# Optimization experiments

Hardware: AMD Instinct MI355X
Metric: run time of the kernel (lower is better)

The kernel has to match this reference:

```python
import jax, jax.numpy as jnp
import numpy as np

EMBED_DIM = 1024
NUM_HEADS = 16
HEAD_DIM = EMBED_DIM // NUM_HEADS


def setup_inputs() -> dict:
    key = jax.random.key(0)
    ks = jax.random.split(key, 9)
    B, N, C = 2, 2048, EMBED_DIM
    s = 1.0 / np.sqrt(C)
    x = jax.random.normal(ks[0], (B, N, C), dtype=jnp.float32)
    Wq = jax.random.uniform(ks[1], (C, C), jnp.float32, -s, s)
    bq = jax.random.uniform(ks[2], (C,), jnp.float32, -s, s)
    Wk = jax.random.uniform(ks[3], (C, C), jnp.float32, -s, s)
    bk = jax.random.uniform(ks[4], (C,), jnp.float32, -s, s)
    Wv = jax.random.uniform(ks[5], (C, C), jnp.float32, -s, s)
    bv = jax.random.uniform(ks[6], (C,), jnp.float32, -s, s)
    Wo = jax.random.uniform(ks[7], (C, C), jnp.float32, -s, s)
    bo = jax.random.uniform(ks[8], (C,), jnp.float32, -s, s)
    return {"x": x, "Wq": Wq, "bq": bq, "Wk": Wk, "bk": bk,
            "Wv": Wv, "bv": bv, "Wo": Wo, "bo": bo}


def reference(x, Wq, bq, Wk, bk, Wv, bv, Wo, bo):
    B, N, C = x.shape
    H, D = NUM_HEADS, HEAD_DIM
    # projections: weights stored as [in, out] (torch Linear applies x @ W.T; here W already transposed)
    q = (x @ Wq + bq).reshape(B, N, H, D).transpose(0, 2, 1, 3)  # [B,H,N,D]
    k = (x @ Wk + bk).reshape(B, N, H, D).transpose(0, 2, 1, 3)
    v = (x @ Wv + bv).reshape(B, N, H, D).transpose(0, 2, 1, 3)
    scores = jnp.einsum('bhnd,bhmd->bhnm', q, k) / jnp.sqrt(jnp.float32(D))
    w = jax.nn.softmax(scores, axis=-1)
    out = jnp.einsum('bhnm,bhmd->bhnd', w, v)  # [B,H,N,D]
    out = out.transpose(0, 2, 1, 3).reshape(B, N, C)
    return out @ Wo + bo
```

## Files before the change

### kernel.cpp

```cpp
#include <hip/hip_runtime.h>

typedef short short4v __attribute__((ext_vector_type(4)));
typedef short short8 __attribute__((ext_vector_type(8)));
typedef unsigned uint4v __attribute__((ext_vector_type(4)));
typedef float floatx4 __attribute__((ext_vector_type(4)));
typedef float floatx16 __attribute__((ext_vector_type(16)));

#define SEQ 2048
#define CDIM 1024
#define NH 16
#define HD 64

__device__ __forceinline__ short f2bf(float f){
  unsigned u = __builtin_bit_cast(unsigned, f);
  u += 0x7fff + ((u >> 16) & 1);
  return (short)(u >> 16);
}
__device__ __forceinline__ float fexp2(float x){
  float r; asm("v_exp_f32 %0, %1" : "=v"(r) : "v"(x)); return r;
}
__device__ __forceinline__ int swz(int row, int k){
  return row*64 + ((((k >> 3) ^ row) & 7) << 3) + (k & 7);
}
__device__ __forceinline__ void gload16(const short* g, short* l){
  __builtin_amdgcn_global_load_lds(
      (const __attribute__((address_space(1))) void*)g,
      (__attribute__((address_space(3))) void*)l, 16, 0, 0);
}

struct PrepArgs { const float* w[4]; short* wT[4]; const float* x; short* xb; };
__global__ __launch_bounds__(256) void prep(PrepArgs pa){
  int z = blockIdx.z, tid = threadIdx.x;
  if(z >= 4){
    int blk = (z-4)*256 + blockIdx.y*16 + blockIdx.x;
    int i = (blk*256 + tid) * 4;
    float4 v = *(const float4*)&pa.x[i];
    short4v o = { f2bf(v.x), f2bf(v.y), f2bf(v.z), f2bf(v.w) };
    *(short4v*)&pa.xb[i] = o;
    return;
  }
  const float* __restrict__ in = pa.w[z];
  short* __restrict__ out = pa.wT[z];
  __shared__ short t[64][68];
  int r0 = blockIdx.y * 64, c0 = blockIdx.x * 64;
  #pragma unroll
  for(int i=0;i<4;i++){
    int id = tid + i*256;
    int r = id >> 4, c4 = (id & 15) * 4;
    float4 v = *(const float4*)&in[(long long)(r0+r)*CDIM + c0 + c4];
    t[r][c4]   = f2bf(v.x); t[r][c4+1] = f2bf(v.y);
    t[r][c4+2] = f2bf(v.z); t[r][c4+3] = f2bf(v.w);
  }
  __syncthreads();
  #pragma unroll
  for(int i=0;i<4;i++){
    int id = tid + i*256;
    int c = id >> 4, r4 = (id & 15) * 4;
    short4v o = { t[r4][c], t[r4+1][c], t[r4+2][c], t[r4+3][c] };
    *(short4v*)&out[(long long)(c0+c)*CDIM + r0 + r4] = o;
  }
}

__global__ __launch_bounds__(256) void transpose64(
    const short* __restrict__ in, short* __restrict__ out,
    long long zs_in, long long zs_out, int ld_in, int ld_out){
  in  += (long long)blockIdx.z * zs_in;
  out += (long long)blockIdx.z * zs_out;
  __shared__ short t[64][72];
  int r0 = blockIdx.y * 64, c0 = blockIdx.x * 64, tid = threadIdx.x;
  #pragma unroll
  for(int i=0;i<2;i++){
    int id = tid + i*256;
    int r = id >> 3, c8 = (id & 7) * 8;
    short8 x = *(const short8*)&in[(long long)(r0+r)*ld_in + c0 + c8];
    #pragma unroll
    for(int j=0;j<8;j++) t[r][c8+j] = x[j];
  }
  __syncthreads();
  #pragma unroll
  for(int i=0;i<2;i++){
    int id = tid + i*256;
    int c = id >> 3, r8 = (id & 7) * 8;
    short8 x;
    #pragma unroll
    for(int j=0;j<8;j++) x[j] = t[r8+j][c];
    *(short8*)&out[(long long)(c0+c)*ld_out + r0 + r8] = x;
  }
}

struct GemmArgs {
  const short* X;
  const short* Wt[3];
  const float* bias[3];
  void* out[3];
  float scale[3];
  int mode;
};

__global__ __launch_bounds__(256,4) void gemm128(GemmArgs ga){
  int z = blockIdx.z;
  const short* __restrict__ X  = ga.X;
  const short* __restrict__ Wt = ga.Wt[z];
  const float* __restrict__ bi = ga.bias[z];

  __shared__ __align__(16) short As[128*64];
  __shared__ __align__(16) short Bs[128*64];
  int tid = threadIdx.x, lane = tid & 63, w = tid >> 6;
  int m0 = blockIdx.x * 128, n0 = blockIdx.y * 128;
  int wr = (w >> 1) * 64, wc = (w & 1) * 64;
  int rsub = lane >> 3;
  int ksw  = (((lane & 7) ^ (lane >> 3)) & 7) << 3;

  const short* gA = X  + (long long)m0 * CDIM;
  const short* gB = Wt + (long long)n0 * CDIM;

  floatx4 acc[4][4];
  #pragma unroll
  for(int m=0;m<4;m++)
    #pragma unroll
    for(int n=0;n<4;n++) acc[m][n] = (floatx4){0.f,0.f,0.f,0.f};

  for(int kt=0; kt<CDIM; kt+=64){
    #pragma unroll
    for(int i=0;i<4;i++){
      int rr = (i*4+w)*8 + rsub;
      gload16(gA + (long long)rr*CDIM + kt + ksw, &As[(i*4+w)*512]);
      gload16(gB + (long long)rr*CDIM + kt + ksw, &Bs[(i*4+w)*512]);
    }
    __syncthreads();
    #pragma unroll
    for(int kk=0;kk<2;kk++){
      int kb = kk*32 + (lane>>4)*8;
      short8 af[4], bfq[4];
      #pragma unroll
      for(int m=0;m<4;m++) af[m]  = *(short8*)&As[swz(wr + m*16 + (lane&15), kb)];
      #pragma unroll
      for(int n=0;n<4;n++) bfq[n] = *(short8*)&Bs[swz(wc + n*16 + (lane&15), kb)];
      __builtin_amdgcn_s_setprio(1);
      #pragma unroll
      for(int m=0;m<4;m++)
        #pragma unroll
        for(int n=0;n<4;n++)
          acc[m][n] = __builtin_amdgcn_mfma_f32_16x16x32_bf16(af[m], bfq[n], acc[m][n], 0,0,0);
      __builtin_amdgcn_s_setprio(0);
    }
    __syncthreads();
  }

  #pragma unroll
  for(int m=0;m<4;m++){
    #pragma unroll
    for(int n=0;n<4;n++){
      int col = n0 + wc + n*16 + (lane & 15);
      float b = bi[col];
      #pragma unroll
      for(int j=0;j<4;j++){
        int row = m0 + wr + m*16 + (lane>>4)*4 + j;
        float r = acc[m][n][j] + b;
        if(ga.mode == 0){
          ((float*)ga.out[z])[(long long)row*CDIM + col] = r;
        } else {
          int bb = row >> 11, nn = row & 2047;
          int hh = col >> 6, dd = col & 63;
          ((short*)ga.out[z])[(long long)(((bb<<4)+hh)*SEQ + nn)*HD + dd] = f2bf(r * ga.scale[z]);
        }
      }
    }
  }
}

__global__ __launch_bounds__(512,4) void attn_fwd(
    const short* __restrict__ q, const short* __restrict__ k,
    const short* __restrict__ vT, short* __restrict__ ao){
  int bh = blockIdx.y;
  int b = bh >> 4, h = bh & 15;
  const short* Q = q  + (long long)bh * SEQ * HD;
  const short* K = k  + (long long)bh * SEQ * HD;
  const short* V = vT + (long long)bh * HD * SEQ;

  __shared__ __align__(16) short Kb[2][64*64];
  __shared__ __align__(16) short Vb[2][64*64];
  int tid = threadIdx.x, lane = tid & 63, w = tid >> 6;
  int wsub = w & 3, half = w >> 2;
  int l31 = lane & 31, hi = lane >> 5;
  int rsub = lane >> 3;
  int ksw  = (((lane & 7) ^ (lane >> 3)) & 7) << 3;
  int q0 = blockIdx.x * 128 + wsub * 32;
  int kvbase = half * (SEQ/2);

  short8 qf[4];
  {
    const short* qp = Q + (long long)(q0 + l31)*HD + hi*8;
    #pragma unroll
    for(int ks=0; ks<4; ks++) qf[ks] = *(const short8*)(qp + ks*16);
  }
  short8 onesf;
  #pragma unroll
  for(int j=0;j<8;j++) onesf[j] = (short)0x3F80;

  floatx16 accO0 = (floatx16)(0.f), accO1 = (floatx16)(0.f);
  floatx16 lacc  = (floatx16)(0.f);

  for(int t=0; t<16; t++){
    int kvn = kvbase + t*64;
    #pragma unroll
    for(int i=0;i<2;i++){
      int r = (i*4+wsub)*8 + rsub;
      gload16(K + (long long)(kvn + r)*HD + ksw, &Kb[half][(i*4+wsub)*512]);
      gload16(V + (long long)r*SEQ + kvn + ksw,  &Vb[half][(i*4+wsub)*512]);
    }
    __syncthreads();

    floatx16 s0 = (floatx16)(0.f), s1 = (floatx16)(0.f);
    __builtin_amdgcn_s_setprio(1);
    #pragma unroll
    for(int ks=0; ks<4; ks++){
      short8 kf0 = *(short8*)&Kb[half][swz(l31,      ks*16 + hi*8)];
      short8 kf1 = *(short8*)&Kb[half][swz(32 + l31, ks*16 + hi*8)];
      s0 = __builtin_amdgcn_mfma_f32_32x32x16_bf16(kf0, qf[ks], s0, 0,0,0);
      s1 = __builtin_amdgcn_mfma_f32_32x32x16_bf16(kf1, qf[ks], s1, 0,0,0);
    }
    __builtin_amdgcn_s_setprio(0);

    float p0[16], p1[16];
    #pragma unroll
    for(int r=0;r<16;r++){ p0[r] = fexp2(s0[r]); p1[r] = fexp2(s1[r]); }

    unsigned c0,c1,c2,c3,c4,c5,c6,c7, d0,d1,d2,d3,d4,d5,d6,d7;
    asm("v_cvt_pk_bf16_f32 %0, %1, %2" : "=v"(c0) : "v"(p0[0]),  "v"(p0[1]));
    asm("v_cvt_pk_bf16_f32 %0, %1, %2" : "=v"(c1) : "v"(p0[2]),  "v"(p0[3]));
    asm("v_cvt_pk_bf16_f32 %0, %1, %2" : "=v"(c2) : "v"(p0[4]),  "v"(p0[5]));
    asm("v_cvt_pk_bf16_f32 %0, %1, %2" : "=v"(c3) : "v"(p0[6]),  "v"(p0[7]));
    asm("v_cvt_pk_bf16_f32 %0, %1, %2" : "=v"(c4) : "v"(p0[8]),  "v"(p0[9]));
    asm("v_cvt_pk_bf16_f32 %0, %1, %2" : "=v"(c5) : "v"(p0[10]), "v"(p0[11]));
    asm("v_cvt_pk_bf16_f32 %0, %1, %2" : "=v"(c6) : "v"(p0[12]), "v"(p0[13]));
    asm("v_cvt_pk_bf16_f32 %0, %1, %2" : "=v"(c7) : "v"(p0[14]), "v"(p0[15]));
    asm("v_cvt_pk_bf16_f32 %0, %1, %2" : "=v"(d0) : "v"(p1[0]),  "v"(p1[1]));
    asm("v_cvt_pk_bf16_f32 %0, %1, %2" : "=v"(d1) : "v"(p1[2]),  "v"(p1[3]));
    asm("v_cvt_pk_bf16_f32 %0, %1, %2" : "=v"(d2) : "v"(p1[4]),  "v"(p1[5]));
    asm("v_cvt_pk_bf16_f32 %0, %1, %2" : "=v"(d3) : "v"(p1[6]),  "v"(p1[7]));
    asm("v_cvt_pk_bf16_f32 %0, %1, %2" : "=v"(d4) : "v"(p1[8]),  "v"(p1[9]));
    asm("v_cvt_pk_bf16_f32 %0, %1, %2" : "=v"(d5) : "v"(p1[10]), "v"(p1[11]));
    asm("v_cvt_pk_bf16_f32 %0, %1, %2" : "=v"(d6) : "v"(p1[12]), "v"(p1[13]));
    asm("v_cvt_pk_bf16_f32 %0, %1, %2" : "=v"(d7) : "v"(p1[14]), "v"(p1[15]));
    asm("v_permlane32_swap_b32 %0, %1" : "+v"(c0), "+v"(c2));
    asm("v_permlane32_swap_b32 %0, %1" : "+v"(c1), "+v"(c3));
    asm("v_permlane32_swap_b32 %0, %1" : "+v"(c4), "+v"(c6));
    asm("v_permlane32_swap_b32 %0, %1" : "+v"(c5), "+v"(c7));
    asm("v_permlane32_swap_b32 %0, %1" : "+v"(d0), "+v"(d2));
    asm("v_permlane32_swap_b32 %0, %1" : "+v"(d1), "+v"(d3));
    asm("v_permlane32_swap_b32 %0, %1" : "+v"(d4), "+v"(d6));
    asm("v_permlane32_swap_b32 %0, %1" : "+v"(d5), "+v"(d7));
    short8 pa[4];
    { uint4v u = {c0,c1,c2,c3}; pa[0] = __builtin_bit_cast(short8, u); }
    { uint4v u = {c4,c5,c6,c7}; pa[1] = __builtin_bit_cast(short8, u); }
    { uint4v u = {d0,d1,d2,d3}; pa[2] = __builtin_bit_cast(short8, u); }
    { uint4v u = {d4,d5,d6,d7}; pa[3] = __builtin_bit_cast(short8, u); }

    __builtin_amdgcn_s_setprio(1);
    #pragma unroll
    for(int ks=0; ks<4; ks++){
      short8 vf0 = *(short8*)&Vb[half][swz(l31,      ks*16 + hi*8)];
      short8 vf1 = *(short8*)&Vb[half][swz(32 + l31, ks*16 + hi*8)];
      accO0 = __builtin_amdgcn_mfma_f32_32x32x16_bf16(pa[ks], vf0, accO0, 0,0,0);
      accO1 = __builtin_amdgcn_mfma_f32_32x32x16_bf16(pa[ks], vf1, accO1, 0,0,0);
      lacc  = __builtin_amdgcn_mfma_f32_32x32x16_bf16(pa[ks], onesf, lacc, 0,0,0);
    }
    __builtin_amdgcn_s_setprio(0);

    __syncthreads();
  }

  float* Ko  = (float*)&Kb[0][0];
  float* VoS = (float*)&Vb[0][0];
  if(half == 1){
    #pragma unroll
    for(int r=0;r<16;r++){
      Ko [(wsub*16 + r)*64 + lane] = accO0[r];
      VoS[(wsub*16 + r)*64 + lane] = accO1[r];
    }
  }
  __syncthreads();
  if(half == 0){
    #pragma unroll
    for(int r=0;r<16;r++){
      accO0[r] += Ko [(wsub*16 + r)*64 + lane];
      accO1[r] += VoS[(wsub*16 + r)*64 + lane];
    }
  }
  __syncthreads();
  if(half == 1){
    #pragma unroll
    for(int r=0;r<16;r++) Ko[(wsub*16 + r)*64 + lane] = lacc[r];
  }
  __syncthreads();
  if(half == 0){
    #pragma unroll
    for(int r=0;r<16;r++){
      int qr = (r&3) + 8*(r>>2) + 4*hi;
      float lnew = lacc[r] + Ko[(wsub*16 + r)*64 + lane];
      float inv = 1.f / lnew;
      long long row = (long long)(b*SEQ + q0 + qr);
      ao[row*CDIM + h*HD + l31]      = f2bf(accO0[r] * inv);
      ao[row*CDIM + h*HD + 32 + l31] = f2bf(accO1[r] * inv);
    }
  }
}

extern "C" void kernel_launch(void* const* d_in, const int* in_sizes, int n_in,
                              void* d_out, int out_size, void* d_ws, size_t ws_size,
                              hipStream_t stream){
  const float* x  = (const float*)d_in[0];
  const float* Wq = (const float*)d_in[1];
  const float* bq = (const float*)d_in[2];
  const float* Wk = (const float*)d_in[3];
  const float* bk = (const float*)d_in[4];
  const float* Wv = (const float*)d_in[5];
  const float* bv = (const float*)d_in[6];
  const float* Wo = (const float*)d_in[7];
  const float* bo = (const float*)d_in[8];
  short* ws = (short*)d_ws;

  const long long M1 = 1048576;
  short* xb  = ws;
  short* wqT = ws + 4*M1;
  short* wkT = ws + 5*M1;
  short* wvT = ws + 6*M1;
  short* woT = ws + 7*M1;
  short* qb  = ws + 8*M1;
  short* kb  = ws + 12*M1;
  short* vb  = ws + 16*M1;
  short* vT  = xb;
  short* ao  = vb;

  dim3 tb(256);
  PrepArgs pp;
  pp.w[0]=Wq; pp.w[1]=Wk; pp.w[2]=Wv; pp.w[3]=Wo;
  pp.wT[0]=wqT; pp.wT[1]=wkT; pp.wT[2]=wvT; pp.wT[3]=woT;
  pp.x = x; pp.xb = xb;
  prep<<<dim3(16,16,20), tb, 0, stream>>>(pp);

  const float QSCALE = 0.125f * 1.4426950408889634f;
  GemmArgs g1;
  g1.X = xb;
  g1.Wt[0]=wqT; g1.Wt[1]=wkT; g1.Wt[2]=wvT;
  g1.bias[0]=bq; g1.bias[1]=bk; g1.bias[2]=bv;
  g1.out[0]=qb; g1.out[1]=kb; g1.out[2]=vb;
  g1.scale[0]=QSCALE; g1.scale[1]=1.f; g1.scale[2]=1.f;
  g1.mode = 1;
  gemm128<<<dim3(32,8,3), tb, 0, stream>>>(g1);

  transpose64<<<dim3(1,32,32), tb, 0, stream>>>(vb, vT, 131072, 131072, 64, 2048);

  attn_fwd<<<dim3(16,32,1), dim3(512), 0, stream>>>(qb, kb, vT, ao);

  GemmArgs g2;
  g2.X = ao;
  g2.Wt[0]=woT; g2.Wt[1]=woT; g2.Wt[2]=woT;
  g2.bias[0]=bo; g2.bias[1]=bo; g2.bias[2]=bo;
  g2.out[0]=d_out; g2.out[1]=d_out; g2.out[2]=d_out;
  g2.scale[0]=1.f; g2.scale[1]=1.f; g2.scale[2]=1.f;
  g2.mode = 0;
  gemm128<<<dim3(32,8,1), tb, 0, stream>>>(g2);
}
```

Before: 119.0 us.

## Fuse V transpose into QKV GEMM epilogue and read head-major attention output

The QKV projection GEMM now writes V directly in transposed [B,H,D,N] layout through a new epilogue mode, so the separate transpose kernel launch is removed. Attention writes its output in head-major [B,H,N,D] layout, reusing the Q buffer, and the output-projection GEMM gains an A-layout flag to gather its input tiles from that layout. This removes one kernel launch and one round trip of V through memory. In exchange, the V epilogue stores are strided across SEQ and poorly coalesced, and the aliasing of AO with Q drops the restrict qualifiers in attention.

```diff
diff --git a/kernel.cpp b/kernel.cpp
--- a/kernel.cpp
+++ b/kernel.cpp
@@ -61,40 +61,14 @@
   }
 }
 
-__global__ __launch_bounds__(256) void transpose64(
-    const short* __restrict__ in, short* __restrict__ out,
-    long long zs_in, long long zs_out, int ld_in, int ld_out){
-  in  += (long long)blockIdx.z * zs_in;
-  out += (long long)blockIdx.z * zs_out;
-  __shared__ short t[64][72];
-  int r0 = blockIdx.y * 64, c0 = blockIdx.x * 64, tid = threadIdx.x;
-  #pragma unroll
-  for(int i=0;i<2;i++){
-    int id = tid + i*256;
-    int r = id >> 3, c8 = (id & 7) * 8;
-    short8 x = *(const short8*)&in[(long long)(r0+r)*ld_in + c0 + c8];
-    #pragma unroll
-    for(int j=0;j<8;j++) t[r][c8+j] = x[j];
-  }
-  __syncthreads();
-  #pragma unroll
-  for(int i=0;i<2;i++){
-    int id = tid + i*256;
-    int c = id >> 3, r8 = (id & 7) * 8;
-    short8 x;
-    #pragma unroll
-    for(int j=0;j<8;j++) x[j] = t[r8+j][c];
-    *(short8*)&out[(long long)(c0+c)*ld_out + r0 + r8] = x;
-  }
-}
-
 struct GemmArgs {
   const short* X;
   const short* Wt[3];
   const float* bias[3];
   void* out[3];
   float scale[3];
-  int mode;
+  int mode[3];
+  int alay;
 };
 
 __global__ __launch_bounds__(256,4) void gemm128(GemmArgs ga){
@@ -102,6 +76,7 @@
   const short* __restrict__ X  = ga.X;
   const short* __restrict__ Wt = ga.Wt[z];
   const float* __restrict__ bi = ga.bias[z];
+  int mode = ga.mode[z];
 
   __shared__ __align__(16) short As[128*64];
   __shared__ __align__(16) short Bs[128*64];
@@ -111,7 +86,6 @@
   int rsub = lane >> 3;
   int ksw  = (((lane & 7) ^ (lane >> 3)) & 7) << 3;
 
-  const short* gA = X  + (long long)m0 * CDIM;
   const short* gB = Wt + (long long)n0 * CDIM;
 
   floatx4 acc[4][4];
@@ -124,7 +98,13 @@
     #pragma unroll
     for(int i=0;i<4;i++){
       int rr = (i*4+w)*8 + rsub;
-      gload16(gA + (long long)rr*CDIM + kt + ksw, &As[(i*4+w)*512]);
+      const short* srcA;
+      if(ga.alay)
+        srcA = X + (long long)(((m0>>11)<<4) + (kt>>6))*131072
+                 + (long long)((m0 & 2047) + rr)*64 + ksw;
+      else
+        srcA = X + (long long)(m0+rr)*CDIM + kt + ksw;
+      gload16(srcA, &As[(i*4+w)*512]);
       gload16(gB + (long long)rr*CDIM + kt + ksw, &Bs[(i*4+w)*512]);
     }
     __syncthreads();
@@ -157,12 +137,14 @@
       for(int j=0;j<4;j++){
         int row = m0 + wr + m*16 + (lane>>4)*4 + j;
         float r = acc[m][n][j] + b;
-        if(ga.mode == 0){
+        int bb = row >> 11, nn = row & 2047;
+        int hh = col >> 6, dd = col & 63;
+        if(mode == 0){
           ((float*)ga.out[z])[(long long)row*CDIM + col] = r;
+        } else if(mode == 1){
+          ((short*)ga.out[z])[(long long)(((bb<<4)+hh)*SEQ + nn)*HD + dd] = f2bf(r * ga.scale[z]);
         } else {
-          int bb = row >> 11, nn = row & 2047;
-          int hh = col >> 6, dd = col & 63;
-          ((short*)ga.out[z])[(long long)(((bb<<4)+hh)*SEQ + nn)*HD + dd] = f2bf(r * ga.scale[z]);
+          ((short*)ga.out[z])[(long long)(((bb<<4)+hh)*HD + dd)*SEQ + nn] = f2bf(r * ga.scale[z]);
         }
       }
     }
@@ -170,13 +152,13 @@
 }
 
 __global__ __launch_bounds__(512,4) void attn_fwd(
-    const short* __restrict__ q, const short* __restrict__ k,
-    const short* __restrict__ vT, short* __restrict__ ao){
+    const short* q, const short* __restrict__ k,
+    const short* __restrict__ vT, short* ao){
   int bh = blockIdx.y;
-  int b = bh >> 4, h = bh & 15;
   const short* Q = q  + (long long)bh * SEQ * HD;
   const short* K = k  + (long long)bh * SEQ * HD;
   const short* V = vT + (long long)bh * HD * SEQ;
+  short* AO = ao + (long long)bh * SEQ * HD;
 
   __shared__ __align__(16) short Kb[2][64*64];
   __shared__ __align__(16) short Vb[2][64*64];
@@ -300,9 +282,9 @@
       int qr = (r&3) + 8*(r>>2) + 4*hi;
       float lnew = lacc[r] + Ko[(wsub*16 + r)*64 + lane];
       float inv = 1.f / lnew;
-      long long row = (long long)(b*SEQ + q0 + qr);
-      ao[row*CDIM + h*HD + l31]      = f2bf(accO0[r] * inv);
-      ao[row*CDIM + h*HD + 32 + l31] = f2bf(accO1[r] * inv);
+      long long rowoff = (long long)(q0 + qr) * HD;
+      AO[rowoff + l31]      = f2bf(accO0[r] * inv);
+      AO[rowoff + 32 + l31] = f2bf(accO1[r] * inv);
     }
   }
 }
@@ -329,9 +311,8 @@
   short* woT = ws + 7*M1;
   short* qb  = ws + 8*M1;
   short* kb  = ws + 12*M1;
-  short* vb  = ws + 16*M1;
-  short* vT  = xb;
-  short* ao  = vb;
+  short* vT  = ws + 16*M1;
+  short* ao  = qb;
 
   dim3 tb(256);
   PrepArgs pp;
@@ -345,12 +326,11 @@
   g1.X = xb;
   g1.Wt[0]=wqT; g1.Wt[1]=wkT; g1.Wt[2]=wvT;
   g1.bias[0]=bq; g1.bias[1]=bk; g1.bias[2]=bv;
-  g1.out[0]=qb; g1.out[1]=kb; g1.out[2]=vb;
+  g1.out[0]=qb; g1.out[1]=kb; g1.out[2]=vT;
   g1.scale[0]=QSCALE; g1.scale[1]=1.f; g1.scale[2]=1.f;
-  g1.mode = 1;
+  g1.mode[0]=1; g1.mode[1]=1; g1.mode[2]=2;
+  g1.alay = 0;
   gemm128<<<dim3(32,8,3), tb, 0, stream>>>(g1);
-
-  transpose64<<<dim3(1,32,32), tb, 0, stream>>>(vb, vT, 131072, 131072, 64, 2048);
 
   attn_fwd<<<dim3(16,32,1), dim3(512), 0, stream>>>(qb, kb, vT, ao);
 
@@ -360,6 +340,7 @@
   g2.bias[0]=bo; g2.bias[1]=bo; g2.bias[2]=bo;
   g2.out[0]=d_out; g2.out[1]=d_out; g2.out[2]=d_out;
   g2.scale[0]=1.f; g2.scale[1]=1.f; g2.scale[2]=1.f;
-  g2.mode = 0;
+  g2.mode[0]=0; g2.mode[1]=0; g2.mode[2]=0;
+  g2.alay = 1;
   gemm128<<<dim3(32,8,1), tb, 0, stream>>>(g2);
 }
```

Result: no change. 120.0 us, median of 2 (+0.8%).
